# Performance work log

Hardware: AMD Instinct MI355X
Metric: run time of the kernel (lower is better)

## Reference

```python
import jax, jax.numpy as jnp
import numpy as np

H = 1024      # LSTM_DIM
D = 1024      # BERT_DIM
VW = 30000    # word vocab
VA = 30       # action vocab
T = 64        # transition steps
S = 512       # BERT memory length


def lstm_cell(x, h, c, Wih, Whh, bih, bhh):
    # torch.nn.LSTMCell math: gates ordered i, f, g, o
    g = x @ Wih.T + bih + h @ Whh.T + bhh
    i, f, gg, o = jnp.split(g, 4, axis=-1)
    c2 = jax.nn.sigmoid(f) * c + jax.nn.sigmoid(i) * jnp.tanh(gg)
    h2 = jax.nn.sigmoid(o) * jnp.tanh(c2)
    return h2, c2


def forward(memory, actions, words,
            term_Wih, term_Whh, term_bih, term_bhh,
            act_Wih, act_Whh, act_bih, act_bhh,
            Wq, bq, Wa1, ba1, Wa2, ba2, Ww1, bw1, Ww2, bw2,
            act_emb, word_emb):
    z = jnp.zeros((1, H), dtype=memory.dtype)

    def step(carry, xs):
        term_h, term_c, act_h, act_c, stack_h = carry
        a_t, w_t = xs
        # predict_action: concat decoder states, dot-attention over BERT memory (no softmax)
        states = jnp.concatenate([term_h, act_h, stack_h], axis=1)     # [1, 3H]
        q = states @ Wq.T + bq                                          # [1, D]
        attn = jnp.einsum('bsd,bd->bs', memory, q)                      # [1, S]
        ctx = jnp.einsum('bs,bsd->bd', attn, memory)                    # [1, D]
        final = jnp.concatenate([states, ctx], axis=1)                  # [1, 3H+D]
        act_logits = jax.nn.relu(final @ Wa1.T + ba1) @ Wa2.T + ba2     # [1, VA]
        word_logits = jax.nn.relu(final @ Ww1.T + bw1) @ Ww2.T + bw2    # [1, VW]
        # do_action: act LSTM step, then SHIFT: word embedding into term LSTM + stack push
        a_e = act_emb[a_t][None, :]
        act_h2, act_c2 = lstm_cell(a_e, act_h, act_c, act_Wih, act_Whh, act_bih, act_bhh)
        w_e = word_emb[w_t][None, :]
        term_h2, term_c2 = lstm_cell(w_e, term_h, term_c, term_Wih, term_Whh, term_bih, term_bhh)
        new_carry = (term_h2, term_c2, act_h2, act_c2, w_e)
        return new_carry, (act_logits[0], word_logits[0])

    carry0 = (z, z, z, z, z)
    _, (act_logits, word_logits) = jax.lax.scan(step, carry0, (actions, words))
    return act_logits, word_logits  # [T, VA], [T, VW]


def setup_inputs() -> dict:
    key = jax.random.key(0)
    ks = jax.random.split(key, 24)
    s = 0.02

    def n(k, shape):
        return jax.random.normal(k, shape, dtype=jnp.float32) * s

    return {
        'memory': jax.random.normal(ks[0], (1, S, D), dtype=jnp.float32),
        'actions': jax.random.randint(ks[1], (T,), 0, VA),
        'words': jax.random.randint(ks[2], (T,), 0, VW),
        'term_Wih': n(ks[3], (4 * H, H)), 'term_Whh': n(ks[4], (4 * H, H)),
        'term_bih': n(ks[5], (4 * H,)), 'term_bhh': n(ks[6], (4 * H,)),
        'act_Wih': n(ks[7], (4 * H, H)), 'act_Whh': n(ks[8], (4 * H, H)),
        'act_bih': n(ks[9], (4 * H,)), 'act_bhh': n(ks[10], (4 * H,)),
        'Wq': n(ks[11], (D, 3 * H)), 'bq': n(ks[12], (D,)),
        'Wa1': n(ks[13], (H, 3 * H + D)), 'ba1': n(ks[14], (H,)),
        'Wa2': n(ks[15], (VA, H)), 'ba2': n(ks[16], (VA,)),
        'Ww1': n(ks[17], (H, 3 * H + D)), 'bw1': n(ks[18], (H,)),
        'Ww2': n(ks[19], (VW, H)), 'bw2': n(ks[20], (VW,)),
        'act_emb': n(ks[21], (VA, H)),
        'word_emb': n(ks[22], (VW, H)),
    }


def reference(memory, actions, words,
              term_Wih, term_Whh, term_bih, term_bhh,
              act_Wih, act_Whh, act_bih, act_bhh,
              Wq, bq, Wa1, ba1, Wa2, ba2, Ww1, bw1, Ww2, bw2,
              act_emb, word_emb):
    return forward(memory, actions, words,
                   term_Wih, term_Whh, term_bih, term_bhh,
                   act_Wih, act_Whh, act_bih, act_bhh,
                   Wq, bq, Wa1, ba1, Wa2, ba2, Ww1, bw1, Ww2, bw2,
                   act_emb, word_emb)
```

## Files before the change

### kernel.cpp

```cpp
#include <hip/hip_runtime.h>

#define H 1024
#define T_STEPS 64
#define S_MEM 512
#define VA 30
#define VW 30000

__device__ __forceinline__ float sigmf(float x) { return 1.f / (1.f + expf(-x)); }

__global__ __launch_bounds__(256) void k_init(
    const int* __restrict__ actions, const int* __restrict__ words,
    const float* __restrict__ act_emb, const float* __restrict__ word_emb,
    float* __restrict__ X_term, float* __restrict__ X_act,
    float* __restrict__ fin, unsigned long long* __restrict__ htag) {
  int b = blockIdx.x, tid = threadIdx.x;
  if (b < T_STEPS) {
    int wi = words[b], ai = actions[b];
    for (int i = tid; i < H; i += 256) {
      float we = word_emb[(size_t)wi * H + i];
      X_term[b * H + i] = we;
      X_act[b * H + i]  = act_emb[(size_t)ai * H + i];
      if (b + 1 < T_STEPS) fin[(size_t)(b + 1) * 4096 + 2048 + i] = we;
    }
    if (b == 0)
      for (int i = tid; i < H; i += 256) fin[2048 + i] = 0.f;
  } else if (b == T_STEPS) {
    for (int i = tid; i < H; i += 256) { fin[i] = 0.f; fin[H + i] = 0.f; }
  } else {
    for (int i = (b - 65) * 256 + tid; i < 64 * 2048; i += 64 * 256) htag[i] = 0ull;
  }
}

template<bool BT>
__global__ __launch_bounds__(256) void k_gemm64(
    const float* __restrict__ A, int lda,
    const float* __restrict__ B, int ldb,
    int N, int K,
    float* __restrict__ Ppart,
    const float* __restrict__ bias, const float* __restrict__ bias2, int relu,
    float* __restrict__ Cfinal, int ldc) {
  __shared__ __align__(16) float As[64 * 64];
  __shared__ __align__(16) float Bs[64 * 64];
  const float4* As4 = (const float4*)As;
  const float4* Bs4 = (const float4*)Bs;
  int tid = threadIdx.x;
  int cidx = tid & 15;
  int ridx = tid >> 4;
  int n0 = blockIdx.x * 64;
  int splitk = gridDim.y;
  int klen = K / splitk;
  int kbeg = blockIdx.y * klen;
  float acc[4][4] = {};

  for (int k0 = kbeg; k0 < kbeg + klen; k0 += 64) {
#pragma unroll
    for (int i = 0; i < 4; ++i) {
      int f = tid + i * 256;
      int rr = f >> 4, km = f & 15;
      float4 v = *(const float4*)&A[(size_t)rr * lda + k0 + km * 4];
      int c2 = ((rr >> 2) ^ km) & 15, p = rr & 3;
      As[(km * 4 + 0) * 64 + c2 * 4 + p] = v.x;
      As[(km * 4 + 1) * 64 + c2 * 4 + p] = v.y;
      As[(km * 4 + 2) * 64 + c2 * 4 + p] = v.z;
      As[(km * 4 + 3) * 64 + c2 * 4 + p] = v.w;
    }
    if (BT) {
#pragma unroll
      for (int i = 0; i < 4; ++i) {
        int f = tid + i * 256;
        int nn = f >> 4, km = f & 15;
        int gn = n0 + nn;
        float4 v = make_float4(0.f, 0.f, 0.f, 0.f);
        if (gn < N) v = *(const float4*)&B[(size_t)gn * ldb + k0 + km * 4];
        int c2 = ((nn >> 2) ^ km) & 15, p = nn & 3;
        Bs[(km * 4 + 0) * 64 + c2 * 4 + p] = v.x;
        Bs[(km * 4 + 1) * 64 + c2 * 4 + p] = v.y;
        Bs[(km * 4 + 2) * 64 + c2 * 4 + p] = v.z;
        Bs[(km * 4 + 3) * 64 + c2 * 4 + p] = v.w;
      }
    } else {
#pragma unroll
      for (int i = 0; i < 4; ++i) {
        int f = tid + i * 256;
        int kr = f >> 4, nq = f & 15;
        int gn = n0 + nq * 4;
        float4 v = make_float4(0.f, 0.f, 0.f, 0.f);
        if (gn < N) v = *(const float4*)&B[(size_t)(k0 + kr) * ldb + gn];
        ((float4*)Bs)[kr * 16 + ((nq ^ (kr >> 2)) & 15)] = v;
      }
    }
    __syncthreads();
#pragma unroll 8
    for (int kk = 0; kk < 64; ++kk) {
      int sw = kk >> 2;
      float4 a4 = As4[kk * 16 + ((ridx ^ sw) & 15)];
      float4 b4 = Bs4[kk * 16 + ((cidx ^ sw) & 15)];
      float av[4] = {a4.x, a4.y, a4.z, a4.w};
      float bv[4] = {b4.x, b4.y, b4.z, b4.w};
#pragma unroll
      for (int i = 0; i < 4; ++i)
#pragma unroll
        for (int j = 0; j < 4; ++j) acc[i][j] += av[i] * bv[j];
    }
    __syncthreads();
  }

  int gcol = n0 + cidx * 4;
  if (splitk > 1) {
    float* P = Ppart + (size_t)blockIdx.y * 64 * N;
    if (gcol < N) {
#pragma unroll
      for (int i = 0; i < 4; ++i) {
        int row = ridx * 4 + i;
        *(float4*)&P[(size_t)row * N + gcol] =
            make_float4(acc[i][0], acc[i][1], acc[i][2], acc[i][3]);
      }
    }
  } else {
    if (gcol < N) {
      float4 bs = bias ? *(const float4*)&bias[gcol] : make_float4(0, 0, 0, 0);
      if (bias2) {
        float4 b2 = *(const float4*)&bias2[gcol];
        bs.x += b2.x; bs.y += b2.y; bs.z += b2.z; bs.w += b2.w;
      }
#pragma unroll
      for (int i = 0; i < 4; ++i) {
        int row = ridx * 4 + i;
        float4 v = make_float4(acc[i][0] + bs.x, acc[i][1] + bs.y,
                               acc[i][2] + bs.z, acc[i][3] + bs.w);
        if (relu) {
          v.x = fmaxf(v.x, 0.f); v.y = fmaxf(v.y, 0.f);
          v.z = fmaxf(v.z, 0.f); v.w = fmaxf(v.w, 0.f);
        }
        *(float4*)&Cfinal[(size_t)row * ldc + gcol] = v;
      }
    }
  }
}

__global__ __launch_bounds__(256) void k_gemm_dual(
    const float* __restrict__ A0, const float* __restrict__ A1, int lda,
    const float* __restrict__ B0, const float* __restrict__ B1, int ldb,
    int N, int K, float* __restrict__ P0, float* __restrict__ P1) {
  __shared__ __align__(16) float As[64 * 64];
  __shared__ __align__(16) float Bs[64 * 64];
  const float4* As4 = (const float4*)As;
  const float4* Bs4 = (const float4*)Bs;
  const float* A = blockIdx.z ? A1 : A0;
  const float* B = blockIdx.z ? B1 : B0;
  float* Pp = blockIdx.z ? P1 : P0;
  int tid = threadIdx.x;
  int cidx = tid & 15;
  int ridx = tid >> 4;
  int n0 = blockIdx.x * 64;
  int klen = K / gridDim.y;
  int kbeg = blockIdx.y * klen;
  float acc[4][4] = {};

  for (int k0 = kbeg; k0 < kbeg + klen; k0 += 64) {
#pragma unroll
    for (int i = 0; i < 4; ++i) {
      int f = tid + i * 256;
      int rr = f >> 4, km = f & 15;
      float4 v = *(const float4*)&A[(size_t)rr * lda + k0 + km * 4];
      int c2 = ((rr >> 2) ^ km) & 15, p = rr & 3;
      As[(km * 4 + 0) * 64 + c2 * 4 + p] = v.x;
      As[(km * 4 + 1) * 64 + c2 * 4 + p] = v.y;
      As[(km * 4 + 2) * 64 + c2 * 4 + p] = v.z;
      As[(km * 4 + 3) * 64 + c2 * 4 + p] = v.w;
    }
#pragma unroll
    for (int i = 0; i < 4; ++i) {
      int f = tid + i * 256;
      int nn = f >> 4, km = f & 15;
      int gn = n0 + nn;
      float4 v = make_float4(0.f, 0.f, 0.f, 0.f);
      if (gn < N) v = *(const float4*)&B[(size_t)gn * ldb + k0 + km * 4];
      int c2 = ((nn >> 2) ^ km) & 15, p = nn & 3;
      Bs[(km * 4 + 0) * 64 + c2 * 4 + p] = v.x;
      Bs[(km * 4 + 1) * 64 + c2 * 4 + p] = v.y;
      Bs[(km * 4 + 2) * 64 + c2 * 4 + p] = v.z;
      Bs[(km * 4 + 3) * 64 + c2 * 4 + p] = v.w;
    }
    __syncthreads();
#pragma unroll 8
    for (int kk = 0; kk < 64; ++kk) {
      int sw = kk >> 2;
      float4 a4 = As4[kk * 16 + ((ridx ^ sw) & 15)];
      float4 b4 = Bs4[kk * 16 + ((cidx ^ sw) & 15)];
      float av[4] = {a4.x, a4.y, a4.z, a4.w};
      float bv[4] = {b4.x, b4.y, b4.z, b4.w};
#pragma unroll
      for (int i = 0; i < 4; ++i)
#pragma unroll
        for (int j = 0; j < 4; ++j) acc[i][j] += av[i] * bv[j];
    }
    __syncthreads();
  }
  int gcol = n0 + cidx * 4;
  float* P = Pp + (size_t)blockIdx.y * 64 * N;
  if (gcol < N) {
#pragma unroll
    for (int i = 0; i < 4; ++i) {
      int row = ridx * 4 + i;
      *(float4*)&P[(size_t)row * N + gcol] =
          make_float4(acc[i][0], acc[i][1], acc[i][2], acc[i][3]);
    }
  }
}

__global__ __launch_bounds__(256) void k_reduce4(
    const float* __restrict__ P, int S, int N,
    const float* __restrict__ bias, const float* __restrict__ bias2, int relu,
    float* __restrict__ out, int ldc) {
  int q = blockIdx.x * 256 + threadIdx.x;
  int total = 64 * N / 4;
  if (q >= total) return;
  int e0 = q * 4;
  int row = e0 / N, col = e0 - row * N;
  float4 v = make_float4(0, 0, 0, 0);
  for (int s = 0; s < S; ++s) {
    float4 p = *(const float4*)&P[(size_t)s * 64 * N + e0];
    v.x += p.x; v.y += p.y; v.z += p.z; v.w += p.w;
  }
  if (bias) {
    float4 b = *(const float4*)&bias[col];
    v.x += b.x; v.y += b.y; v.z += b.z; v.w += b.w;
  }
  if (bias2) {
    float4 b = *(const float4*)&bias2[col];
    v.x += b.x; v.y += b.y; v.z += b.z; v.w += b.w;
  }
  if (relu) {
    v.x = fmaxf(v.x, 0.f); v.y = fmaxf(v.y, 0.f);
    v.z = fmaxf(v.z, 0.f); v.w = fmaxf(v.w, 0.f);
  }
  *(float4*)&out[(size_t)row * ldc + col] = v;
}

__global__ __launch_bounds__(256) void k_reduce_dual(
    const float* __restrict__ P0, const float* __restrict__ P1, int S, int N,
    const float* __restrict__ ba0, const float* __restrict__ ba1,
    const float* __restrict__ bb0, const float* __restrict__ bb1,
    float* __restrict__ o0, float* __restrict__ o1, int relu) {
  const float* P = blockIdx.y ? P1 : P0;
  const float* bias = blockIdx.y ? ba1 : ba0;
  const float* bias2 = blockIdx.y ? bb1 : bb0;
  float* out = blockIdx.y ? o1 : o0;
  int q = blockIdx.x * 256 + threadIdx.x;
  int total = 64 * N / 4;
  if (q >= total) return;
  int e0 = q * 4;
  int col = e0 % N;
  float4 v = make_float4(0, 0, 0, 0);
  for (int s = 0; s < S; ++s) {
    float4 p = *(const float4*)&P[(size_t)s * 64 * N + e0];
    v.x += p.x; v.y += p.y; v.z += p.z; v.w += p.w;
  }
  if (bias) {
    float4 b = *(const float4*)&bias[col];
    v.x += b.x; v.y += b.y; v.z += b.z; v.w += b.w;
  }
  if (bias2) {
    float4 b = *(const float4*)&bias2[col];
    v.x += b.x; v.y += b.y; v.z += b.z; v.w += b.w;
  }
  if (relu) {
    v.x = fmaxf(v.x, 0.f); v.y = fmaxf(v.y, 0.f);
    v.z = fmaxf(v.z, 0.f); v.w = fmaxf(v.w, 0.f);
  }
  *(float4*)&out[e0] = v;
}

__global__ __launch_bounds__(256, 1) void k_recur(
    const float* __restrict__ Whh_term, const float* __restrict__ Whh_act,
    const float* __restrict__ xg_term, const float* __restrict__ xg_act,
    float* __restrict__ fin, unsigned long long* __restrict__ htag) {
  __shared__ float hs[32 * 36];
  __shared__ float xgs[63 * 32];
  int b = blockIdx.x, tid = threadIdx.x;
  int lstm = b >> 7, k0 = (b & 127) * 8;
  const float* Whh = lstm ? Whh_act : Whh_term;
  const float* xg  = lstm ? xg_act : xg_term;
  int d = tid >> 5, p = tid & 31;

  float wreg[128];
#pragma unroll
  for (int g = 0; g < 4; ++g) {
    const float* wrow = Whh + (size_t)(g * 1024 + k0 + d) * 1024 + p * 32;
#pragma unroll
    for (int i = 0; i < 32; i += 4) {
      float4 v = *(const float4*)(wrow + i);
      wreg[g * 32 + i]     = v.x; wreg[g * 32 + i + 1] = v.y;
      wreg[g * 32 + i + 2] = v.z; wreg[g * 32 + i + 3] = v.w;
    }
  }
#pragma unroll
  for (int i = 0; i < 128; ++i) asm volatile("" : "+v"(wreg[i]));

  for (int i = tid; i < 63 * 32; i += 256) {
    int rr = i & 31;
    xgs[i] = xg[(size_t)(i >> 5) * 4096 + (rr >> 3) * 1024 + k0 + (rr & 7)];
  }
  float c_loc = 0.f;

  for (int t = 0; t < 63; ++t) {
    if (t > 0) {
      const unsigned long long* src = htag + (size_t)t * 2048 + lstm * 1024;
#pragma unroll
      for (int j = 0; j < 4; ++j) {
        int idx = tid + j * 256;
        unsigned long long v = __hip_atomic_load(&src[idx], __ATOMIC_RELAXED,
                                                 __HIP_MEMORY_SCOPE_AGENT);
        while ((unsigned)(v >> 32) != (unsigned)t) {
          __builtin_amdgcn_s_sleep(1);
          v = __hip_atomic_load(&src[idx], __ATOMIC_RELAXED, __HIP_MEMORY_SCOPE_AGENT);
        }
        hs[(idx >> 5) * 36 + (idx & 31)] = __uint_as_float((unsigned)v);
      }
    } else {
#pragma unroll
      for (int j = 0; j < 4; ++j) {
        int idx = tid + j * 256;
        hs[(idx >> 5) * 36 + (idx & 31)] = 0.f;
      }
    }
    __syncthreads();

    const float* hp = hs + p * 36;
    float s0 = 0.f, s1 = 0.f, s2 = 0.f, s3 = 0.f;
#pragma unroll
    for (int i = 0; i < 32; i += 4) {
      float4 hv = *(const float4*)&hp[i];
      s0 += wreg[i] * hv.x + wreg[i + 1] * hv.y + wreg[i + 2] * hv.z + wreg[i + 3] * hv.w;
      s1 += wreg[32 + i] * hv.x + wreg[33 + i] * hv.y + wreg[34 + i] * hv.z + wreg[35 + i] * hv.w;
      s2 += wreg[64 + i] * hv.x + wreg[65 + i] * hv.y + wreg[66 + i] * hv.z + wreg[67 + i] * hv.w;
      s3 += wreg[96 + i] * hv.x + wreg[97 + i] * hv.y + wreg[98 + i] * hv.z + wreg[99 + i] * hv.w;
    }
#pragma unroll
    for (int m = 1; m <= 16; m <<= 1) {
      s0 += __shfl_xor(s0, m); s1 += __shfl_xor(s1, m);
      s2 += __shfl_xor(s2, m); s3 += __shfl_xor(s3, m);
    }
    if (p == 0) {
      float gi = s0 + xgs[t * 32 + d];
      float gf = s1 + xgs[t * 32 + 8 + d];
      float gg = s2 + xgs[t * 32 + 16 + d];
      float go = s3 + xgs[t * 32 + 24 + d];
      float c2 = sigmf(gf) * c_loc + sigmf(gi) * tanhf(gg);
      float h2 = sigmf(go) * tanhf(c2);
      c_loc = c2;
      fin[(size_t)(t + 1) * 4096 + lstm * 1024 + k0 + d] = h2;
      __hip_atomic_store(&htag[(size_t)(t + 1) * 2048 + lstm * 1024 + k0 + d],
                         (((unsigned long long)(t + 1)) << 32) |
                             (unsigned long long)__float_as_uint(h2),
                         __ATOMIC_RELAXED, __HIP_MEMORY_SCOPE_AGENT);
    }
    __syncthreads();
  }
}

__global__ __launch_bounds__(256) void k_actlog(
    const float* __restrict__ ha, const float* __restrict__ Wa2,
    const float* __restrict__ ba2, float* __restrict__ out) {
  int t = blockIdx.x, tid = threadIdx.x;
  int v = tid >> 3, p = tid & 7;
  float sum = 0.f;
  if (v < VA) {
    const float* a  = ha + (size_t)t * 1024 + p * 128;
    const float* wr = Wa2 + (size_t)v * 1024 + p * 128;
#pragma unroll 8
    for (int i = 0; i < 128; i += 4) {
      float4 av = *(const float4*)(a + i);
      float4 wv = *(const float4*)(wr + i);
      sum += av.x * wv.x + av.y * wv.y + av.z * wv.z + av.w * wv.w;
    }
  }
  sum += __shfl_xor(sum, 1);
  sum += __shfl_xor(sum, 2);
  sum += __shfl_xor(sum, 4);
  if (p == 0 && v < VA) out[(size_t)t * VA + v] = sum + ba2[v];
}

extern "C" void kernel_launch(void* const* d_in, const int* in_sizes, int n_in,
                              void* d_out, int out_size, void* d_ws, size_t ws_size,
                              hipStream_t stream) {
  const float* memory   = (const float*)d_in[0];
  const int*   actions  = (const int*)d_in[1];
  const int*   words    = (const int*)d_in[2];
  const float* term_Wih = (const float*)d_in[3];
  const float* term_Whh = (const float*)d_in[4];
  const float* term_bih = (const float*)d_in[5];
  const float* term_bhh = (const float*)d_in[6];
  const float* act_Wih  = (const float*)d_in[7];
  const float* act_Whh  = (const float*)d_in[8];
  const float* act_bih  = (const float*)d_in[9];
  const float* act_bhh  = (const float*)d_in[10];
  const float* Wq  = (const float*)d_in[11];
  const float* bq  = (const float*)d_in[12];
  const float* Wa1 = (const float*)d_in[13];
  const float* ba1 = (const float*)d_in[14];
  const float* Wa2 = (const float*)d_in[15];
  const float* ba2 = (const float*)d_in[16];
  const float* Ww1 = (const float*)d_in[17];
  const float* bw1 = (const float*)d_in[18];
  const float* Ww2 = (const float*)d_in[19];
  const float* bw2 = (const float*)d_in[20];
  const float* act_emb  = (const float*)d_in[21];
  const float* word_emb = (const float*)d_in[22];
  float* out = (float*)d_out;

  float* w       = (float*)d_ws;
  float* X_term  = w;
  float* X_act   = X_term + 65536;
  float* xg_term = X_act + 65536;
  float* xg_act  = xg_term + 262144;
  float* fin     = xg_act + 262144;
  float* qbuf    = fin + 262144;
  float* attn    = qbuf + 65536;
  float* ha      = attn + 32768;
  float* hw      = ha + 65536;
  unsigned long long* htag = (unsigned long long*)(hw + 65536);
  float* P       = (float*)(htag + 64 * 2048);

  size_t base_fl = (size_t)(P - w);
  int wsplit = (ws_size >= (base_fl + 2ull * 64 * VW + 1024) * 4) ? 2 : 1;

  k_init<<<129, 256, 0, stream>>>(actions, words, act_emb, word_emb,
                                  X_term, X_act, fin, htag);

  k_gemm_dual<<<dim3(64, 2, 2), 256, 0, stream>>>(
      X_term, X_act, 1024, term_Wih, act_Wih, 1024, 4096, 1024, P, P + 524288);
  k_reduce_dual<<<dim3(256, 2), 256, 0, stream>>>(
      P, P + 524288, 2, 4096, term_bih, act_bih, term_bhh, act_bhh, xg_term, xg_act, 0);

  k_recur<<<256, 256, 0, stream>>>(term_Whh, act_Whh, xg_term, xg_act, fin, htag);

  k_gemm64<true><<<dim3(16, 8), 256, 0, stream>>>(fin, 4096, Wq, 3072, 1024, 3072,
                                                  P, nullptr, nullptr, 0, nullptr, 0);
  k_reduce4<<<64, 256, 0, stream>>>(P, 8, 1024, bq, nullptr, 0, qbuf, 1024);

  k_gemm64<true><<<dim3(8, 8), 256, 0, stream>>>(qbuf, 1024, memory, 1024, 512, 1024,
                                                 P, nullptr, nullptr, 0, nullptr, 0);
  k_reduce4<<<32, 256, 0, stream>>>(P, 8, 512, nullptr, nullptr, 0, attn, 512);

  k_gemm64<false><<<dim3(16, 8), 256, 0, stream>>>(attn, 512, memory, 1024, 1024, 512,
                                                   P, nullptr, nullptr, 0, nullptr, 0);
  k_reduce4<<<64, 256, 0, stream>>>(P, 8, 1024, nullptr, nullptr, 0, fin + 3072, 4096);

  k_gemm_dual<<<dim3(16, 8, 2), 256, 0, stream>>>(
      fin, fin, 4096, Wa1, Ww1, 4096, 1024, 4096, P, P + 524288);
  k_reduce_dual<<<dim3(64, 2), 256, 0, stream>>>(
      P, P + 524288, 8, 1024, ba1, bw1, nullptr, nullptr, ha, hw, 1);

  k_actlog<<<64, 256, 0, stream>>>(ha, Wa2, ba2, out);

  if (wsplit == 2) {
    k_gemm64<true><<<dim3(469, 2), 256, 0, stream>>>(hw, 1024, Ww2, 1024, VW, 1024,
                                                     P, nullptr, nullptr, 0, nullptr, 0);
    k_reduce4<<<1875, 256, 0, stream>>>(P, 2, VW, bw2, nullptr, 0, out + 1920, VW);
  } else {
    k_gemm64<true><<<dim3(469, 1), 256, 0, stream>>>(hw, 1024, Ww2, 1024, VW, 1024,
                                                     nullptr, bw2, nullptr, 0, out + 1920, VW);
  }
}
```

Measured before the change: 492.3 us.

## Widen recurrent LSTM blocks to 512 threads and double-buffer hidden state

The persistent recurrent kernel now runs 512 threads per block, so each thread keeps 64 weight registers instead of 128, and the dot-product reduction spans a full 64-lane wave. The hidden-state shared buffer is double-buffered, which removes the second barrier per timestep. Spin-waits lose their sleep, so each thread polls two entries in tight loops. The aim is shorter per-step latency on the serial 63-step chain, at the cost of more polling traffic and a wider shuffle reduction.

```diff
diff --git a/kernel.cpp b/kernel.cpp
--- a/kernel.cpp
+++ b/kernel.cpp
@@ -272,73 +272,75 @@
   *(float4*)&out[e0] = v;
 }
 
-__global__ __launch_bounds__(256, 1) void k_recur(
+__global__ __launch_bounds__(512, 2) void k_recur(
     const float* __restrict__ Whh_term, const float* __restrict__ Whh_act,
     const float* __restrict__ xg_term, const float* __restrict__ xg_act,
     float* __restrict__ fin, unsigned long long* __restrict__ htag) {
-  __shared__ float hs[32 * 36];
+  __shared__ float hs[2][1024];
   __shared__ float xgs[63 * 32];
   int b = blockIdx.x, tid = threadIdx.x;
   int lstm = b >> 7, k0 = (b & 127) * 8;
   const float* Whh = lstm ? Whh_act : Whh_term;
   const float* xg  = lstm ? xg_act : xg_term;
-  int d = tid >> 5, p = tid & 31;
-
-  float wreg[128];
+  int d = tid >> 6, p = tid & 63;
+
+  float wreg[64];
 #pragma unroll
   for (int g = 0; g < 4; ++g) {
-    const float* wrow = Whh + (size_t)(g * 1024 + k0 + d) * 1024 + p * 32;
-#pragma unroll
-    for (int i = 0; i < 32; i += 4) {
+    const float* wrow = Whh + (size_t)((g << 10) + k0 + d) * 1024 + p * 16;
+#pragma unroll
+    for (int i = 0; i < 16; i += 4) {
       float4 v = *(const float4*)(wrow + i);
-      wreg[g * 32 + i]     = v.x; wreg[g * 32 + i + 1] = v.y;
-      wreg[g * 32 + i + 2] = v.z; wreg[g * 32 + i + 3] = v.w;
-    }
-  }
-#pragma unroll
-  for (int i = 0; i < 128; ++i) asm volatile("" : "+v"(wreg[i]));
-
-  for (int i = tid; i < 63 * 32; i += 256) {
+      wreg[g * 16 + i]     = v.x; wreg[g * 16 + i + 1] = v.y;
+      wreg[g * 16 + i + 2] = v.z; wreg[g * 16 + i + 3] = v.w;
+    }
+  }
+#pragma unroll
+  for (int i = 0; i < 64; ++i) asm volatile("" : "+v"(wreg[i]));
+
+  for (int i = tid; i < 63 * 32; i += 512) {
     int rr = i & 31;
-    xgs[i] = xg[(size_t)(i >> 5) * 4096 + (rr >> 3) * 1024 + k0 + (rr & 7)];
+    xgs[i] = xg[(size_t)(i >> 5) * 4096 + (size_t)(rr >> 3) * 1024 + k0 + (rr & 7)];
   }
   float c_loc = 0.f;
 
   for (int t = 0; t < 63; ++t) {
+    float* hb = hs[t & 1];
     if (t > 0) {
       const unsigned long long* src = htag + (size_t)t * 2048 + lstm * 1024;
-#pragma unroll
-      for (int j = 0; j < 4; ++j) {
-        int idx = tid + j * 256;
-        unsigned long long v = __hip_atomic_load(&src[idx], __ATOMIC_RELAXED,
-                                                 __HIP_MEMORY_SCOPE_AGENT);
-        while ((unsigned)(v >> 32) != (unsigned)t) {
-          __builtin_amdgcn_s_sleep(1);
-          v = __hip_atomic_load(&src[idx], __ATOMIC_RELAXED, __HIP_MEMORY_SCOPE_AGENT);
-        }
-        hs[(idx >> 5) * 36 + (idx & 31)] = __uint_as_float((unsigned)v);
-      }
+      unsigned long long v0 = __hip_atomic_load(&src[tid], __ATOMIC_RELAXED,
+                                                __HIP_MEMORY_SCOPE_AGENT);
+      unsigned long long v1 = __hip_atomic_load(&src[tid + 512], __ATOMIC_RELAXED,
+                                                __HIP_MEMORY_SCOPE_AGENT);
+      while ((unsigned)(v0 >> 32) != (unsigned)t)
+        v0 = __hip_atomic_load(&src[tid], __ATOMIC_RELAXED, __HIP_MEMORY_SCOPE_AGENT);
+      while ((unsigned)(v1 >> 32) != (unsigned)t)
+        v1 = __hip_atomic_load(&src[tid + 512], __ATOMIC_RELAXED, __HIP_MEMORY_SCOPE_AGENT);
+      hb[tid]       = __uint_as_float((unsigned)v0);
+      hb[tid + 512] = __uint_as_float((unsigned)v1);
     } else {
-#pragma unroll
-      for (int j = 0; j < 4; ++j) {
-        int idx = tid + j * 256;
-        hs[(idx >> 5) * 36 + (idx & 31)] = 0.f;
-      }
+      hb[tid] = 0.f;
+      hb[tid + 512] = 0.f;
     }
     __syncthreads();
 
-    const float* hp = hs + p * 36;
-    float s0 = 0.f, s1 = 0.f, s2 = 0.f, s3 = 0.f;
-#pragma unroll
-    for (int i = 0; i < 32; i += 4) {
-      float4 hv = *(const float4*)&hp[i];
-      s0 += wreg[i] * hv.x + wreg[i + 1] * hv.y + wreg[i + 2] * hv.z + wreg[i + 3] * hv.w;
-      s1 += wreg[32 + i] * hv.x + wreg[33 + i] * hv.y + wreg[34 + i] * hv.z + wreg[35 + i] * hv.w;
-      s2 += wreg[64 + i] * hv.x + wreg[65 + i] * hv.y + wreg[66 + i] * hv.z + wreg[67 + i] * hv.w;
-      s3 += wreg[96 + i] * hv.x + wreg[97 + i] * hv.y + wreg[98 + i] * hv.z + wreg[99 + i] * hv.w;
-    }
-#pragma unroll
-    for (int m = 1; m <= 16; m <<= 1) {
+    const float4* hp = (const float4*)(hb + (p << 4));
+    float4 h0 = hp[0], h1 = hp[1], h2q = hp[2], h3 = hp[3];
+    float s0, s1, s2, s3;
+    {
+      float hv[16] = {h0.x, h0.y, h0.z, h0.w, h1.x, h1.y, h1.z, h1.w,
+                      h2q.x, h2q.y, h2q.z, h2q.w, h3.x, h3.y, h3.z, h3.w};
+      s0 = s1 = s2 = s3 = 0.f;
+#pragma unroll
+      for (int i = 0; i < 16; ++i) {
+        s0 += wreg[i] * hv[i];
+        s1 += wreg[16 + i] * hv[i];
+        s2 += wreg[32 + i] * hv[i];
+        s3 += wreg[48 + i] * hv[i];
+      }
+    }
+#pragma unroll
+    for (int m = 1; m <= 32; m <<= 1) {
       s0 += __shfl_xor(s0, m); s1 += __shfl_xor(s1, m);
       s2 += __shfl_xor(s2, m); s3 += __shfl_xor(s3, m);
     }
@@ -356,7 +358,6 @@
                              (unsigned long long)__float_as_uint(h2),
                          __ATOMIC_RELAXED, __HIP_MEMORY_SCOPE_AGENT);
     }
-    __syncthreads();
   }
 }
 
@@ -434,7 +435,7 @@
   k_reduce_dual<<<dim3(256, 2), 256, 0, stream>>>(
       P, P + 524288, 2, 4096, term_bih, act_bih, term_bhh, act_bhh, xg_term, xg_act, 0);
 
-  k_recur<<<256, 256, 0, stream>>>(term_Whh, act_Whh, xg_term, xg_act, fin, htag);
+  k_recur<<<256, 512, 0, stream>>>(term_Whh, act_Whh, xg_term, xg_act, fin, htag);
 
   k_gemm64<true><<<dim3(16, 8), 256, 0, stream>>>(fin, 4096, Wq, 3072, 1024, 3072,
                                                   P, nullptr, nullptr, 0, nullptr, 0);
```

After: 516.2 us. 1.05x slower.

## Fold split-K reductions into consumer GEMM loads and merge action logits into word GEMM

Applied to the files above, without the earlier changes.

Removes the separate split-K reduction kernels by summing the partial products while the next kernel loads its A tiles. This applies to the input-gate partials and biases in the recurrence, the query partials in the attention GEMM, the attention partials in the context GEMM, and the context partials in the Wa1/Ww1 GEMM. The action-logit computation is moved into an extra block of the word-logit GEMM, and the workspace is reorganised to reuse buffers. This cuts kernel launches and intermediate round trips to memory, but the consumer loads become redundant, since each partial is re-read by every column block. The context GEMM now uses only 32 blocks.

```diff
diff --git a/kernel.cpp b/kernel.cpp
--- a/kernel.cpp
+++ b/kernel.cpp
@@ -6,13 +6,15 @@
 #define VA 30
 #define VW 30000
 
+typedef unsigned long long u64;
+
 __device__ __forceinline__ float sigmf(float x) { return 1.f / (1.f + expf(-x)); }
 
 __global__ __launch_bounds__(256) void k_init(
     const int* __restrict__ actions, const int* __restrict__ words,
     const float* __restrict__ act_emb, const float* __restrict__ word_emb,
     float* __restrict__ X_term, float* __restrict__ X_act,
-    float* __restrict__ fin, unsigned long long* __restrict__ htag) {
+    float* __restrict__ fin, u64* __restrict__ htag) {
   int b = blockIdx.x, tid = threadIdx.x;
   if (b < T_STEPS) {
     int wi = words[b], ai = actions[b];
@@ -141,7 +143,8 @@
 __global__ __launch_bounds__(256) void k_gemm_dual(
     const float* __restrict__ A0, const float* __restrict__ A1, int lda,
     const float* __restrict__ B0, const float* __restrict__ B1, int ldb,
-    int N, int K, float* __restrict__ P0, float* __restrict__ P1) {
+    int N, int K, float* __restrict__ P0, float* __restrict__ P1,
+    const float* __restrict__ APc, int kb) {
   __shared__ __align__(16) float As[64 * 64];
   __shared__ __align__(16) float Bs[64 * 64];
   const float4* As4 = (const float4*)As;
@@ -162,7 +165,15 @@
     for (int i = 0; i < 4; ++i) {
       int f = tid + i * 256;
       int rr = f >> 4, km = f & 15;
-      float4 v = *(const float4*)&A[(size_t)rr * lda + k0 + km * 4];
+      float4 v;
+      if (k0 >= kb) {
+        int kc = k0 - kb + km * 4;
+        float4 a = *(const float4*)&APc[(size_t)rr * 1024 + kc];
+        float4 c = *(const float4*)&APc[65536 + (size_t)rr * 1024 + kc];
+        v = make_float4(a.x + c.x, a.y + c.y, a.z + c.z, a.w + c.w);
+      } else {
+        v = *(const float4*)&A[(size_t)rr * lda + k0 + km * 4];
+      }
       int c2 = ((rr >> 2) ^ km) & 15, p = rr & 3;
       As[(km * 4 + 0) * 64 + c2 * 4 + p] = v.x;
       As[(km * 4 + 1) * 64 + c2 * 4 + p] = v.y;
@@ -209,43 +220,144 @@
   }
 }
 
-__global__ __launch_bounds__(256) void k_reduce4(
-    const float* __restrict__ P, int S, int N,
-    const float* __restrict__ bias, const float* __restrict__ bias2, int relu,
-    float* __restrict__ out, int ldc) {
-  int q = blockIdx.x * 256 + threadIdx.x;
-  int total = 64 * N / 4;
-  if (q >= total) return;
-  int e0 = q * 4;
-  int row = e0 / N, col = e0 - row * N;
-  float4 v = make_float4(0, 0, 0, 0);
-  for (int s = 0; s < S; ++s) {
-    float4 p = *(const float4*)&P[(size_t)s * 64 * N + e0];
-    v.x += p.x; v.y += p.y; v.z += p.z; v.w += p.w;
-  }
-  if (bias) {
-    float4 b = *(const float4*)&bias[col];
-    v.x += b.x; v.y += b.y; v.z += b.z; v.w += b.w;
-  }
-  if (bias2) {
-    float4 b = *(const float4*)&bias2[col];
-    v.x += b.x; v.y += b.y; v.z += b.z; v.w += b.w;
-  }
-  if (relu) {
-    v.x = fmaxf(v.x, 0.f); v.y = fmaxf(v.y, 0.f);
-    v.z = fmaxf(v.z, 0.f); v.w = fmaxf(v.w, 0.f);
-  }
-  *(float4*)&out[(size_t)row * ldc + col] = v;
+__global__ __launch_bounds__(256) void k_attn(
+    const float* __restrict__ Pq, const float* __restrict__ bq,
+    const float* __restrict__ mem, float* __restrict__ Pa) {
+  __shared__ __align__(16) float As[64 * 64];
+  __shared__ __align__(16) float Bs[64 * 64];
+  const float4* As4 = (const float4*)As;
+  const float4* Bs4 = (const float4*)Bs;
+  int tid = threadIdx.x;
+  int cidx = tid & 15;
+  int ridx = tid >> 4;
+  int n0 = blockIdx.x * 64;
+  int kbeg = blockIdx.y * 128;
+  float acc[4][4] = {};
+
+  for (int k0 = kbeg; k0 < kbeg + 128; k0 += 64) {
+#pragma unroll
+    for (int i = 0; i < 4; ++i) {
+      int f = tid + i * 256;
+      int rr = f >> 4, km = f & 15;
+      int col = k0 + km * 4;
+      float4 v = *(const float4*)&bq[col];
+#pragma unroll
+      for (int s = 0; s < 8; ++s) {
+        float4 p = *(const float4*)&Pq[(size_t)s * 65536 + (size_t)rr * 1024 + col];
+        v.x += p.x; v.y += p.y; v.z += p.z; v.w += p.w;
+      }
+      int c2 = ((rr >> 2) ^ km) & 15, p = rr & 3;
+      As[(km * 4 + 0) * 64 + c2 * 4 + p] = v.x;
+      As[(km * 4 + 1) * 64 + c2 * 4 + p] = v.y;
+      As[(km * 4 + 2) * 64 + c2 * 4 + p] = v.z;
+      As[(km * 4 + 3) * 64 + c2 * 4 + p] = v.w;
+    }
+#pragma unroll
+    for (int i = 0; i < 4; ++i) {
+      int f = tid + i * 256;
+      int nn = f >> 4, km = f & 15;
+      float4 v = *(const float4*)&mem[(size_t)(n0 + nn) * 1024 + k0 + km * 4];
+      int c2 = ((nn >> 2) ^ km) & 15, p = nn & 3;
+      Bs[(km * 4 + 0) * 64 + c2 * 4 + p] = v.x;
+      Bs[(km * 4 + 1) * 64 + c2 * 4 + p] = v.y;
+      Bs[(km * 4 + 2) * 64 + c2 * 4 + p] = v.z;
+      Bs[(km * 4 + 3) * 64 + c2 * 4 + p] = v.w;
+    }
+    __syncthreads();
+#pragma unroll 8
+    for (int kk = 0; kk < 64; ++kk) {
+      int sw = kk >> 2;
+      float4 a4 = As4[kk * 16 + ((ridx ^ sw) & 15)];
+      float4 b4 = Bs4[kk * 16 + ((cidx ^ sw) & 15)];
+      float av[4] = {a4.x, a4.y, a4.z, a4.w};
+      float bv[4] = {b4.x, b4.y, b4.z, b4.w};
+#pragma unroll
+      for (int i = 0; i < 4; ++i)
+#pragma unroll
+        for (int j = 0; j < 4; ++j) acc[i][j] += av[i] * bv[j];
+    }
+    __syncthreads();
+  }
+  int gcol = n0 + cidx * 4;
+  float* P = Pa + (size_t)blockIdx.y * 64 * 512;
+#pragma unroll
+  for (int i = 0; i < 4; ++i) {
+    int row = ridx * 4 + i;
+    *(float4*)&P[(size_t)row * 512 + gcol] =
+        make_float4(acc[i][0], acc[i][1], acc[i][2], acc[i][3]);
+  }
+}
+
+__global__ __launch_bounds__(256) void k_ctx(
+    const float* __restrict__ Pa, const float* __restrict__ mem,
+    float* __restrict__ Pc) {
+  __shared__ __align__(16) float As[64 * 64];
+  __shared__ __align__(16) float Bs[64 * 64];
+  const float4* As4 = (const float4*)As;
+  const float4* Bs4 = (const float4*)Bs;
+  int tid = threadIdx.x;
+  int cidx = tid & 15;
+  int ridx = tid >> 4;
+  int n0 = blockIdx.x * 64;
+  int kbeg = blockIdx.y * 256;
+  float acc[4][4] = {};
+
+  for (int k0 = kbeg; k0 < kbeg + 256; k0 += 64) {
+#pragma unroll
+    for (int i = 0; i < 4; ++i) {
+      int f = tid + i * 256;
+      int rr = f >> 4, km = f & 15;
+      int col = k0 + km * 4;
+      float4 v = make_float4(0.f, 0.f, 0.f, 0.f);
+#pragma unroll
+      for (int s = 0; s < 8; ++s) {
+        float4 p = *(const float4*)&Pa[(size_t)s * 32768 + (size_t)rr * 512 + col];
+        v.x += p.x; v.y += p.y; v.z += p.z; v.w += p.w;
+      }
+      int c2 = ((rr >> 2) ^ km) & 15, p = rr & 3;
+      As[(km * 4 + 0) * 64 + c2 * 4 + p] = v.x;
+      As[(km * 4 + 1) * 64 + c2 * 4 + p] = v.y;
+      As[(km * 4 + 2) * 64 + c2 * 4 + p] = v.z;
+      As[(km * 4 + 3) * 64 + c2 * 4 + p] = v.w;
+    }
+#pragma unroll
+    for (int i = 0; i < 4; ++i) {
+      int f = tid + i * 256;
+      int kr = f >> 4, nq = f & 15;
+      float4 v = *(const float4*)&mem[(size_t)(k0 + kr) * 1024 + n0 + nq * 4];
+      ((float4*)Bs)[kr * 16 + ((nq ^ (kr >> 2)) & 15)] = v;
+    }
+    __syncthreads();
+#pragma unroll 8
+    for (int kk = 0; kk < 64; ++kk) {
+      int sw = kk >> 2;
+      float4 a4 = As4[kk * 16 + ((ridx ^ sw) & 15)];
+      float4 b4 = Bs4[kk * 16 + ((cidx ^ sw) & 15)];
+      float av[4] = {a4.x, a4.y, a4.z, a4.w};
+      float bv[4] = {b4.x, b4.y, b4.z, b4.w};
+#pragma unroll
+      for (int i = 0; i < 4; ++i)
+#pragma unroll
+        for (int j = 0; j < 4; ++j) acc[i][j] += av[i] * bv[j];
+    }
+    __syncthreads();
+  }
+  int gcol = n0 + cidx * 4;
+  float* P = Pc + (size_t)blockIdx.y * 64 * 1024;
+#pragma unroll
+  for (int i = 0; i < 4; ++i) {
+    int row = ridx * 4 + i;
+    *(float4*)&P[(size_t)row * 1024 + gcol] =
+        make_float4(acc[i][0], acc[i][1], acc[i][2], acc[i][3]);
+  }
 }
 
 __global__ __launch_bounds__(256) void k_reduce_dual(
     const float* __restrict__ P0, const float* __restrict__ P1, int S, int N,
     const float* __restrict__ ba0, const float* __restrict__ ba1,
-    const float* __restrict__ bb0, const float* __restrict__ bb1,
     float* __restrict__ o0, float* __restrict__ o1, int relu) {
   const float* P = blockIdx.y ? P1 : P0;
   const float* bias = blockIdx.y ? ba1 : ba0;
-  const float* bias2 = blockIdx.y ? bb1 : bb0;
   float* out = blockIdx.y ? o1 : o0;
   int q = blockIdx.x * 256 + threadIdx.x;
   int total = 64 * N / 4;
@@ -261,10 +373,6 @@
     float4 b = *(const float4*)&bias[col];
     v.x += b.x; v.y += b.y; v.z += b.z; v.w += b.w;
   }
-  if (bias2) {
-    float4 b = *(const float4*)&bias2[col];
-    v.x += b.x; v.y += b.y; v.z += b.z; v.w += b.w;
-  }
   if (relu) {
     v.x = fmaxf(v.x, 0.f); v.y = fmaxf(v.y, 0.f);
     v.z = fmaxf(v.z, 0.f); v.w = fmaxf(v.w, 0.f);
@@ -272,16 +380,38 @@
   *(float4*)&out[e0] = v;
 }
 
+__global__ __launch_bounds__(256) void k_reduce4(
+    const float* __restrict__ P, int S, int N,
+    const float* __restrict__ bias, float* __restrict__ out) {
+  int q = blockIdx.x * 256 + threadIdx.x;
+  int total = 64 * N / 4;
+  if (q >= total) return;
+  int e0 = q * 4;
+  int col = e0 % N;
+  float4 v = make_float4(0, 0, 0, 0);
+  for (int s = 0; s < S; ++s) {
+    float4 p = *(const float4*)&P[(size_t)s * 64 * N + e0];
+    v.x += p.x; v.y += p.y; v.z += p.z; v.w += p.w;
+  }
+  float4 b = *(const float4*)&bias[col];
+  v.x += b.x; v.y += b.y; v.z += b.z; v.w += b.w;
+  *(float4*)&out[e0] = v;
+}
+
 __global__ __launch_bounds__(256, 1) void k_recur(
     const float* __restrict__ Whh_term, const float* __restrict__ Whh_act,
-    const float* __restrict__ xg_term, const float* __restrict__ xg_act,
-    float* __restrict__ fin, unsigned long long* __restrict__ htag) {
+    const float* __restrict__ Pxg_term, const float* __restrict__ Pxg_act,
+    const float* __restrict__ bih_t, const float* __restrict__ bhh_t,
+    const float* __restrict__ bih_a, const float* __restrict__ bhh_a,
+    float* __restrict__ fin, u64* __restrict__ htag) {
   __shared__ float hs[32 * 36];
   __shared__ float xgs[63 * 32];
   int b = blockIdx.x, tid = threadIdx.x;
   int lstm = b >> 7, k0 = (b & 127) * 8;
   const float* Whh = lstm ? Whh_act : Whh_term;
-  const float* xg  = lstm ? xg_act : xg_term;
+  const float* Pxg = lstm ? Pxg_act : Pxg_term;
+  const float* bih = lstm ? bih_a : bih_t;
+  const float* bhh = lstm ? bhh_a : bhh_t;
   int d = tid >> 5, p = tid & 31;
 
   float wreg[128];
@@ -299,25 +429,40 @@
   for (int i = 0; i < 128; ++i) asm volatile("" : "+v"(wreg[i]));
 
   for (int i = tid; i < 63 * 32; i += 256) {
-    int rr = i & 31;
-    xgs[i] = xg[(size_t)(i >> 5) * 4096 + (rr >> 3) * 1024 + k0 + (rr & 7)];
+    int rr = i & 31, t2 = i >> 5;
+    int row2 = (rr >> 3) * 1024 + k0 + (rr & 7);
+    xgs[i] = Pxg[(size_t)t2 * 4096 + row2] + Pxg[262144 + (size_t)t2 * 4096 + row2] +
+             bih[row2] + bhh[row2];
   }
   float c_loc = 0.f;
 
   for (int t = 0; t < 63; ++t) {
     if (t > 0) {
-      const unsigned long long* src = htag + (size_t)t * 2048 + lstm * 1024;
-#pragma unroll
-      for (int j = 0; j < 4; ++j) {
-        int idx = tid + j * 256;
-        unsigned long long v = __hip_atomic_load(&src[idx], __ATOMIC_RELAXED,
-                                                 __HIP_MEMORY_SCOPE_AGENT);
-        while ((unsigned)(v >> 32) != (unsigned)t) {
-          __builtin_amdgcn_s_sleep(1);
-          v = __hip_atomic_load(&src[idx], __ATOMIC_RELAXED, __HIP_MEMORY_SCOPE_AGENT);
-        }
-        hs[(idx >> 5) * 36 + (idx & 31)] = __uint_as_float((unsigned)v);
-      }
+      const u64* src = htag + (size_t)t * 2048 + lstm * 1024;
+      u64 v0 = __hip_atomic_load(&src[tid], __ATOMIC_RELAXED, __HIP_MEMORY_SCOPE_AGENT);
+      u64 v1 = __hip_atomic_load(&src[tid + 256], __ATOMIC_RELAXED, __HIP_MEMORY_SCOPE_AGENT);
+      u64 v2 = __hip_atomic_load(&src[tid + 512], __ATOMIC_RELAXED, __HIP_MEMORY_SCOPE_AGENT);
+      u64 v3 = __hip_atomic_load(&src[tid + 768], __ATOMIC_RELAXED, __HIP_MEMORY_SCOPE_AGENT);
+      while ((unsigned)(v0 >> 32) != (unsigned)t) {
+        __builtin_amdgcn_s_sleep(1);
+        v0 = __hip_atomic_load(&src[tid], __ATOMIC_RELAXED, __HIP_MEMORY_SCOPE_AGENT);
+      }
+      while ((unsigned)(v1 >> 32) != (unsigned)t) {
+        __builtin_amdgcn_s_sleep(1);
+        v1 = __hip_atomic_load(&src[tid + 256], __ATOMIC_RELAXED, __HIP_MEMORY_SCOPE_AGENT);
+      }
+      while ((unsigned)(v2 >> 32) != (unsigned)t) {
+        __builtin_amdgcn_s_sleep(1);
+        v2 = __hip_atomic_load(&src[tid + 512], __ATOMIC_RELAXED, __HIP_MEMORY_SCOPE_AGENT);
+      }
+      while ((unsigned)(v3 >> 32) != (unsigned)t) {
+        __builtin_amdgcn_s_sleep(1);
+        v3 = __hip_atomic_load(&src[tid + 768], __ATOMIC_RELAXED, __HIP_MEMORY_SCOPE_AGENT);
+      }
+      hs[((tid) >> 5) * 36 + (tid & 31)]         = __uint_as_float((unsigned)v0);
+      hs[((tid + 256) >> 5) * 36 + (tid & 31)]   = __uint_as_float((unsigned)v1);
+      hs[((tid + 512) >> 5) * 36 + (tid & 31)]   = __uint_as_float((unsigned)v2);
+      hs[((tid + 768) >> 5) * 36 + (tid & 31)]   = __uint_as_float((unsigned)v3);
     } else {
 #pragma unroll
       for (int j = 0; j < 4; ++j) {
@@ -352,34 +497,114 @@
       c_loc = c2;
       fin[(size_t)(t + 1) * 4096 + lstm * 1024 + k0 + d] = h2;
       __hip_atomic_store(&htag[(size_t)(t + 1) * 2048 + lstm * 1024 + k0 + d],
-                         (((unsigned long long)(t + 1)) << 32) |
-                             (unsigned long long)__float_as_uint(h2),
+                         (((u64)(t + 1)) << 32) | (u64)__float_as_uint(h2),
                          __ATOMIC_RELAXED, __HIP_MEMORY_SCOPE_AGENT);
     }
     __syncthreads();
   }
 }
 
-__global__ __launch_bounds__(256) void k_actlog(
+__global__ __launch_bounds__(256) void k_word(
+    const float* __restrict__ hw, const float* __restrict__ Ww2,
+    const float* __restrict__ bw2, float* __restrict__ Pword, float* __restrict__ outw,
     const float* __restrict__ ha, const float* __restrict__ Wa2,
-    const float* __restrict__ ba2, float* __restrict__ out) {
-  int t = blockIdx.x, tid = threadIdx.x;
-  int v = tid >> 3, p = tid & 7;
-  float sum = 0.f;
-  if (v < VA) {
-    const float* a  = ha + (size_t)t * 1024 + p * 128;
-    const float* wr = Wa2 + (size_t)v * 1024 + p * 128;
+    const float* __restrict__ ba2, float* __restrict__ outa) {
+  int tid = threadIdx.x;
+  if (blockIdx.x == 469) {
+    if (blockIdx.y != 0) return;
+    int tt = tid >> 2, pp = tid & 3;
+    const float* a = ha + (size_t)tt * 1024 + pp * 256;
+    for (int v = 0; v < VA; ++v) {
+      const float* wr = Wa2 + (size_t)v * 1024 + pp * 256;
+      float sum = 0.f;
 #pragma unroll 8
-    for (int i = 0; i < 128; i += 4) {
-      float4 av = *(const float4*)(a + i);
-      float4 wv = *(const float4*)(wr + i);
-      sum += av.x * wv.x + av.y * wv.y + av.z * wv.z + av.w * wv.w;
-    }
-  }
-  sum += __shfl_xor(sum, 1);
-  sum += __shfl_xor(sum, 2);
-  sum += __shfl_xor(sum, 4);
-  if (p == 0 && v < VA) out[(size_t)t * VA + v] = sum + ba2[v];
+      for (int i = 0; i < 256; i += 4) {
+        float4 av = *(const float4*)(a + i);
+        float4 wv = *(const float4*)(wr + i);
+        sum += av.x * wv.x + av.y * wv.y + av.z * wv.z + av.w * wv.w;
+      }
+      sum += __shfl_xor(sum, 1);
+      sum += __shfl_xor(sum, 2);
+      if (pp == 0) outa[(size_t)tt * VA + v] = sum + ba2[v];
+    }
+    return;
+  }
+  __shared__ __align__(16) float As[64 * 64];
+  __shared__ __align__(16) float Bs[64 * 64];
+  const float4* As4 = (const float4*)As;
+  const float4* Bs4 = (const float4*)Bs;
+  int cidx = tid & 15;
+  int ridx = tid >> 4;
+  int n0 = blockIdx.x * 64;
+  int splitk = gridDim.y;
+  int klen = 1024 / splitk;
+  int kbeg = blockIdx.y * klen;
+  float acc[4][4] = {};
+
+  for (int k0 = kbeg; k0 < kbeg + klen; k0 += 64) {
+#pragma unroll
+    for (int i = 0; i < 4; ++i) {
+      int f = tid + i * 256;
+      int rr = f >> 4, km = f & 15;
+      float4 v = *(const float4*)&hw[(size_t)rr * 1024 + k0 + km * 4];
+      int c2 = ((rr >> 2) ^ km) & 15, p = rr & 3;
+      As[(km * 4 + 0) * 64 + c2 * 4 + p] = v.x;
+      As[(km * 4 + 1) * 64 + c2 * 4 + p] = v.y;
+      As[(km * 4 + 2) * 64 + c2 * 4 + p] = v.z;
+      As[(km * 4 + 3) * 64 + c2 * 4 + p] = v.w;
+    }
+#pragma unroll
+    for (int i = 0; i < 4; ++i) {
+      int f = tid + i * 256;
+      int nn = f >> 4, km = f & 15;
+      int gn = n0 + nn;
+      float4 v = make_float4(0.f, 0.f, 0.f, 0.f);
+      if (gn < VW) v = *(const float4*)&Ww2[(size_t)gn * 1024 + k0 + km * 4];
+      int c2 = ((nn >> 2) ^ km) & 15, p = nn & 3;
+      Bs[(km * 4 + 0) * 64 + c2 * 4 + p] = v.x;
+      Bs[(km * 4 + 1) * 64 + c2 * 4 + p] = v.y;
+      Bs[(km * 4 + 2) * 64 + c2 * 4 + p] = v.z;
+      Bs[(km * 4 + 3) * 64 + c2 * 4 + p] = v.w;
+    }
+    __syncthreads();
+#pragma unroll 8
+    for (int kk = 0; kk < 64; ++kk) {
+      int sw = kk >> 2;
+      float4 a4 = As4[kk * 16 + ((ridx ^ sw) & 15)];
+      float4 b4 = Bs4[kk * 16 + ((cidx ^ sw) & 15)];
+      float av[4] = {a4.x, a4.y, a4.z, a4.w};
+      float bv[4] = {b4.x, b4.y, b4.z, b4.w};
+#pragma unroll
+      for (int i = 0; i < 4; ++i)
+#pragma unroll
+        for (int j = 0; j < 4; ++j) acc[i][j] += av[i] * bv[j];
+    }
+    __syncthreads();
+  }
+
+  int gcol = n0 + cidx * 4;
+  if (splitk > 1) {
+    float* P = Pword + (size_t)blockIdx.y * 64 * VW;
+    if (gcol < VW) {
+#pragma unroll
+      for (int i = 0; i < 4; ++i) {
+        int row = ridx * 4 + i;
+        *(float4*)&P[(size_t)row * VW + gcol] =
+            make_float4(acc[i][0], acc[i][1], acc[i][2], acc[i][3]);
+      }
+    }
+  } else {
+    if (gcol < VW) {
+      float4 bs = *(const float4*)&bw2[gcol];
+#pragma unroll
+      for (int i = 0; i < 4; ++i) {
+        int row = ridx * 4 + i;
+        *(float4*)&outw[(size_t)row * VW + gcol] =
+            make_float4(acc[i][0] + bs.x, acc[i][1] + bs.y,
+                        acc[i][2] + bs.z, acc[i][3] + bs.w);
+      }
+    }
+  }
 }
 
 extern "C" void kernel_launch(void* const* d_in, const int* in_sizes, int n_in,
@@ -410,57 +635,44 @@
   const float* word_emb = (const float*)d_in[22];
   float* out = (float*)d_out;
 
-  float* w       = (float*)d_ws;
-  float* X_term  = w;
-  float* X_act   = X_term + 65536;
-  float* xg_term = X_act + 65536;
-  float* xg_act  = xg_term + 262144;
-  float* fin     = xg_act + 262144;
-  float* qbuf    = fin + 262144;
-  float* attn    = qbuf + 65536;
-  float* ha      = attn + 32768;
-  float* hw      = ha + 65536;
-  unsigned long long* htag = (unsigned long long*)(hw + 65536);
-  float* P       = (float*)(htag + 64 * 2048);
-
-  size_t base_fl = (size_t)(P - w);
-  int wsplit = (ws_size >= (base_fl + 2ull * 64 * VW + 1024) * 4) ? 2 : 1;
+  float* w      = (float*)d_ws;
+  float* fin    = w;
+  u64*   htag   = (u64*)(w + 262144);
+  float* Pa     = (float*)htag;
+  float* X_term = w + 524288;
+  float* X_act  = w + 589824;
+  float* Pc     = X_term;
+  float* ha     = w + 655360;
+  float* hw     = w + 720896;
+  float* arena  = w + 786432;
+
+  int wsplit = (ws_size >= (size_t)(786432 + 2 * 64 * VW) * 4) ? 2 : 1;
 
   k_init<<<129, 256, 0, stream>>>(actions, words, act_emb, word_emb,
                                   X_term, X_act, fin, htag);
 
   k_gemm_dual<<<dim3(64, 2, 2), 256, 0, stream>>>(
-      X_term, X_act, 1024, term_Wih, act_Wih, 1024, 4096, 1024, P, P + 524288);
-  k_reduce_dual<<<dim3(256, 2), 256, 0, stream>>>(
-      P, P + 524288, 2, 4096, term_bih, act_bih, term_bhh, act_bhh, xg_term, xg_act, 0);
-
-  k_recur<<<256, 256, 0, stream>>>(term_Whh, act_Whh, xg_term, xg_act, fin, htag);
+      X_term, X_act, 1024, term_Wih, act_Wih, 1024, 4096, 1024,
+      arena, arena + 524288, nullptr, 1 << 30);
+
+  k_recur<<<256, 256, 0, stream>>>(term_Whh, act_Whh, arena, arena + 524288,
+                                   term_bih, term_bhh, act_bih, act_bhh, fin, htag);
 
   k_gemm64<true><<<dim3(16, 8), 256, 0, stream>>>(fin, 4096, Wq, 3072, 1024, 3072,
-                                                  P, nullptr, nullptr, 0, nullptr, 0);
-  k_reduce4<<<64, 256, 0, stream>>>(P, 8, 1024, bq, nullptr, 0, qbuf, 1024);
-
-  k_gemm64<true><<<dim3(8, 8), 256, 0, stream>>>(qbuf, 1024, memory, 1024, 512, 1024,
-                                                 P, nullptr, nullptr, 0, nullptr, 0);
-  k_reduce4<<<32, 256, 0, stream>>>(P, 8, 512, nullptr, nullptr, 0, attn, 512);
-
-  k_gemm64<false><<<dim3(16, 8), 256, 0, stream>>>(attn, 512, memory, 1024, 1024, 512,
-                                                   P, nullptr, nullptr, 0, nullptr, 0);
-  k_reduce4<<<64, 256, 0, stream>>>(P, 8, 1024, nullptr, nullptr, 0, fin + 3072, 4096);
+                                                  arena, nullptr, nullptr, 0, nullptr, 0);
+
+  k_attn<<<dim3(8, 8), 256, 0, stream>>>(arena, bq, memory, Pa);
+
+  k_ctx<<<dim3(16, 2), 256, 0, stream>>>(Pa, memory, Pc);
 
   k_gemm_dual<<<dim3(16, 8, 2), 256, 0, stream>>>(
-      fin, fin, 4096, Wa1, Ww1, 4096, 1024, 4096, P, P + 524288);
+      fin, fin, 4096, Wa1, Ww1, 4096, 1024, 4096,
+      arena, arena + 524288, Pc, 3072);
   k_reduce_dual<<<dim3(64, 2), 256, 0, stream>>>(
-      P, P + 524288, 8, 1024, ba1, bw1, nullptr, nullptr, ha, hw, 1);
-
-  k_actlog<<<64, 256, 0, stream>>>(ha, Wa2, ba2, out);
-
-  if (wsplit == 2) {
-    k_gemm64<true><<<dim3(469, 2), 256, 0, stream>>>(hw, 1024, Ww2, 1024, VW, 1024,
-                                                     P, nullptr, nullptr, 0, nullptr, 0);
-    k_reduce4<<<1875, 256, 0, stream>>>(P, 2, VW, bw2, nullptr, 0, out + 1920, VW);
-  } else {
-    k_gemm64<true><<<dim3(469, 1), 256, 0, stream>>>(hw, 1024, Ww2, 1024, VW, 1024,
-                                                     nullptr, bw2, nullptr, 0, out + 1920, VW);
-  }
-}
+      arena, arena + 524288, 8, 1024, ba1, bw1, ha, hw, 1);
+
+  k_word<<<dim3(470, wsplit), 256, 0, stream>>>(
+      hw, Ww2, bw2, arena, out + 1920, ha, Wa2, ba2, out);
+  if (wsplit == 2)
+    k_reduce4<<<1875, 256, 0, stream>>>(arena, 2, VW, bw2, out + 1920);
+}
```

Result: slower. 817.1 us (+66.0%).
